# Optimization experiments

Hardware: AMD Instinct MI355X
Metric: run time of the kernel (lower is better)

Reference implementation:

```python
import jax, jax.numpy as jnp
import numpy as np

B, T, C = 1, 2048, 2048
H = 16
DN, DR, DV = 128, 64, 128          # qk_nope_head_dim, qk_rope_head_dim, v_head_dim
QKD = DN + DR                      # 192
RQ, RKV = 1536, 512                # q_lora_rank, kv_lora_rank
EPS = 1e-6
SCALE = QKD ** -0.5


def rmsnorm(v, w):
    return v * jax.lax.rsqrt(jnp.mean(v * v, axis=-1, keepdims=True) + EPS) * w


def rope(x, freqs):
    # x: (B, T, H, d), freqs: (T, d//2) angles. Consecutive-pair complex rotation
    # matching torch view_as_complex(x.reshape(..., -1, 2)) * freqs.
    cos = jnp.cos(freqs)[None, :, None, :]
    sin = jnp.sin(freqs)[None, :, None, :]
    xp = x.reshape(*x.shape[:-1], -1, 2)
    xr, xi = xp[..., 0], xp[..., 1]
    outr = xr * cos - xi * sin
    outi = xr * sin + xi * cos
    return jnp.stack([outr, outi], axis=-1).reshape(x.shape)


def setup_inputs() -> dict:
    key = jax.random.key(0)
    ks = jax.random.split(key, 8)
    s = 0.02
    pos = jnp.arange(T, dtype=jnp.float32)
    inv = 1.0 / (10000.0 ** (jnp.arange(0, DR, 2, dtype=jnp.float32) / DR))  # (DR/2,)
    freqs = pos[:, None] * inv[None, :]  # (T, DR/2) rotation angles
    return {
        "x": jax.random.normal(ks[0], (B, T, C), jnp.float32),
        "freqs": freqs,
        "wq_a": jax.random.normal(ks[1], (RQ, C), jnp.float32) * s,
        "bq_a": jnp.zeros((RQ,), jnp.float32),
        "q_norm_w": jnp.ones((RQ,), jnp.float32),
        "wq_b": jax.random.normal(ks[2], (H * QKD, RQ), jnp.float32) * s,
        "bq_b": jnp.zeros((H * QKD,), jnp.float32),
        "wkv_a": jax.random.normal(ks[3], (RKV + DR, C), jnp.float32) * s,
        "bkv_a": jnp.zeros((RKV + DR,), jnp.float32),
        "kv_norm_w": jnp.ones((RKV,), jnp.float32),
        "wkv_b": jax.random.normal(ks[4], (H * (DN + DV), RKV), jnp.float32) * s,
        "bkv_b": jnp.zeros((H * (DN + DV),), jnp.float32),
        "wo": jax.random.normal(ks[5], (C, C), jnp.float32) * s,
        "bo": jnp.zeros((C,), jnp.float32),
        "prefill": 1,
        "cache_pos": 0,
    }


def reference(x, freqs, wq_a, bq_a, q_norm_w, wq_b, bq_b, wkv_a, bkv_a,
              kv_norm_w, wkv_b, bkv_b, wo, bo, prefill, cache_pos):
    # --- low-rank Q projection ---
    q_lat = rmsnorm(x @ wq_a.T + bq_a, q_norm_w)                 # (B,T,RQ)
    q = (q_lat @ wq_b.T + bq_b).reshape(B, T, H, QKD)
    q_nope, q_pe = q[..., :DN], q[..., DN:]
    q_pe = rope(q_pe, freqs)

    # --- low-rank KV projection ---
    kvpe = x @ wkv_a.T + bkv_a                                   # (B,T,RKV+DR)
    kv_lat, k_pe = kvpe[..., :RKV], kvpe[..., RKV:]
    k_pe = rope(k_pe[:, :, None, :], freqs)                      # (B,T,1,DR)
    kvb = (rmsnorm(kv_lat, kv_norm_w) @ wkv_b.T + bkv_b).reshape(B, T, H, DN + DV)
    k_nope, v = kvb[..., :DN], kvb[..., DN:]

    q = jnp.concatenate([q_nope, q_pe], axis=-1)                 # (B,T,H,QKD)
    k = jnp.concatenate([k_nope, jnp.broadcast_to(k_pe, (B, T, H, DR))], axis=-1)

    # --- causal SDPA (prefill: cache holds exactly the current T tokens) ---
    scores = jnp.einsum('bthd,bshd->bhts', q, k) * SCALE         # (B,H,T,T)
    mask = jnp.tril(jnp.ones((T, T), dtype=bool))
    scores = jnp.where(mask, scores, -jnp.inf)
    att = jax.nn.softmax(scores, axis=-1)
    y = jnp.einsum('bhts,bshd->bthd', att, v).reshape(B, T, C)
    return y @ wo.T + bo
```

## Files before the change

kernel.cpp:

```cpp
#include <hip/hip_runtime.h>
#include <hip/hip_bf16.h>


#define T_DIM 2048
#define H_DIM 16
#define SCALE_F 0.07216878364870322f
#define EPS_F 1e-6f
#define NEG_INF (-3.402823466e38f)

typedef __attribute__((ext_vector_type(8))) short short8;
typedef __attribute__((ext_vector_type(4))) float f32x4;
typedef __attribute__((address_space(3))) char lds_char;
typedef const __attribute__((address_space(1))) char glb_char;

__device__ inline void st_out(float* p, float v) { *p = v; }
__device__ inline void st_out(__hip_bfloat16* p, float v) { *p = __float2bfloat16(v); }

__global__ void cast_bf16_kernel(const float* __restrict__ src,
                                 __hip_bfloat16* __restrict__ dst,
                                 int n4_src, int n4_dst) {
    int i = blockIdx.x * 256 + threadIdx.x;
    if (i >= n4_dst) return;
    float4 v = make_float4(0.f, 0.f, 0.f, 0.f);
    if (i < n4_src) v = ((const float4*)src)[i];
    dst[4 * i + 0] = __float2bfloat16(v.x);
    dst[4 * i + 1] = __float2bfloat16(v.y);
    dst[4 * i + 2] = __float2bfloat16(v.z);
    dst[4 * i + 3] = __float2bfloat16(v.w);
}

__global__ void megacast_kernel(const float* __restrict__ x,
                                const float* __restrict__ wq_a,
                                const float* __restrict__ wkv_a,
                                const float* __restrict__ wq_b,
                                const float* __restrict__ bq_a,
                                const float* __restrict__ bkv_a,
                                __hip_bfloat16* __restrict__ x_bf,
                                __hip_bfloat16* __restrict__ A1,
                                __hip_bfloat16* __restrict__ A2,
                                float* __restrict__ bias_ab) {
    const int i = blockIdx.x * 256 + threadIdx.x;
    float4 v = make_float4(0.f, 0.f, 0.f, 0.f);
    __hip_bfloat16* dst;
    if (i < 1048576) {
        v = ((const float4*)x)[i];            dst = x_bf + 4 * (size_t)i;
    } else if (i < 1835008) {
        int k = i - 1048576;
        v = ((const float4*)wq_a)[k];         dst = A1 + 4 * (size_t)k;
    } else if (i < 2162688) {
        int k = i - 1835008;
        if (k < 294912) v = ((const float4*)wkv_a)[k];
        dst = A1 + (size_t)(786432 + k) * 4;
    } else if (i < 3342336) {
        int k = i - 2162688;
        v = ((const float4*)wq_b)[k];         dst = A2 + 4 * (size_t)k;
    } else if (i < 3342880) {
        int k = i - 3342336;
        float4 b = make_float4(0.f, 0.f, 0.f, 0.f);
        if (k < 384) b = ((const float4*)bq_a)[k];
        else if (k < 528) b = ((const float4*)bkv_a)[k - 384];
        ((float4*)bias_ab)[k] = b;
        return;
    } else return;
    dst[0] = __float2bfloat16(v.x);
    dst[1] = __float2bfloat16(v.y);
    dst[2] = __float2bfloat16(v.z);
    dst[3] = __float2bfloat16(v.w);
}

template <typename OT, bool ROPE>
__global__ __launch_bounds__(512) void gemm_mfma_kernel(
    const __hip_bfloat16* __restrict__ A, int lda,
    const __hip_bfloat16* __restrict__ W, int ldw,
    const float* __restrict__ bias,
    OT* __restrict__ C, int ldc,
    float* __restrict__ C2, int ldc2, int splitN, int K,
    const float* __restrict__ freqs) {
    __shared__ __hip_bfloat16 As[2][128 * 64];
    __shared__ __hip_bfloat16 Bs[2][128 * 64];
    const int tid = threadIdx.x;
    const int w = tid >> 6, lane = tid & 63, qd = lane >> 4, lx = lane & 15;

    const int nwg = gridDim.x * gridDim.y;
    const int o = blockIdx.y * gridDim.x + blockIdx.x;
    const int qx = nwg >> 3, rx = nwg & 7;
    const int xcd = o & 7, idx = o >> 3;
    const int neu = (xcd < rx ? xcd * (qx + 1) : rx * (qx + 1) + (xcd - rx) * qx) + idx;
    const int rowB = (neu / gridDim.x) * 128, colB = (neu % gridDim.x) * 128;

    const int wr = (w >> 1) * 32, wc = (w & 1) * 64;

    f32x4 acc[2][4];
#pragma unroll
    for (int i = 0; i < 2; ++i)
#pragma unroll
        for (int j = 0; j < 4; ++j) acc[i][j] = (f32x4)(0.f);

    auto stage = [&](int buf, int k0) {
#pragma unroll
        for (int it = 0; it < 2; ++it) {
            const int g = tid + it * 512;
            const int row = g >> 3, s = g & 7;
            const int sc = (s ^ (row & 7)) * 8;
            const __hip_bfloat16* ga = A + (size_t)(rowB + row) * lda + k0 + sc;
            __builtin_amdgcn_global_load_lds((glb_char*)ga,
                (lds_char*)((char*)&As[buf][0] + (size_t)g * 16), 16, 0, 0);
            const __hip_bfloat16* gb = W + (size_t)(colB + row) * ldw + k0 + sc;
            __builtin_amdgcn_global_load_lds((glb_char*)gb,
                (lds_char*)((char*)&Bs[buf][0] + (size_t)g * 16), 16, 0, 0);
        }
    };

    stage(0, 0);
    __syncthreads();
    int cur = 0;
    const int swz = (lx & 7) << 4;
    for (int k0 = 0; k0 < K; k0 += 64) {
        if (k0 + 64 < K) stage(cur ^ 1, k0 + 64);

#pragma unroll
        for (int kk = 0; kk < 2; ++kk) {
            short8 a[2], b[4];
#pragma unroll
            for (int rt = 0; rt < 2; ++rt)
                a[rt] = *(const short8*)((char*)&As[cur][0]
                    + (size_t)(wr + rt * 16 + lx) * 128 + ((kk * 64 + qd * 16) ^ swz));
#pragma unroll
            for (int ct = 0; ct < 4; ++ct)
                b[ct] = *(const short8*)((char*)&Bs[cur][0]
                    + (size_t)(wc + ct * 16 + lx) * 128 + ((kk * 64 + qd * 16) ^ swz));
#pragma unroll
            for (int rt = 0; rt < 2; ++rt)
#pragma unroll
                for (int ct = 0; ct < 4; ++ct)
                    acc[rt][ct] = __builtin_amdgcn_mfma_f32_16x16x32_bf16(a[rt], b[ct], acc[rt][ct], 0, 0, 0);
        }
        __syncthreads();
        cur ^= 1;
    }

    const bool second = (C2 != nullptr) && (colB >= splitN);
#pragma unroll
    for (int rt = 0; rt < 2; ++rt)
#pragma unroll
        for (int j = 0; j < 4; ++j) {
            const int row = rowB + wr + rt * 16 + 4 * qd + j;
#pragma unroll
            for (int ct = 0; ct < 4; ++ct) {
                const int col = colB + wc + ct * 16 + lx;
                float v = acc[rt][ct][j] + bias[col];
                if constexpr (ROPE) {
                    const float pv = __shfl_xor(v, 1);
                    const int dm = col % 192;
                    if (dm >= 128) {
                        const int ii = (dm - 128) >> 1;
                        const float f = freqs[row * 32 + ii];
                        const float cc = cosf(f), ss = sinf(f);
                        v = (lane & 1) ? (pv * ss + v * cc)
                                       : (v * cc - pv * ss);
                    }
                }
                if (second) C2[(size_t)row * ldc2 + (col - splitN)] = v;
                else        st_out(&C[(size_t)row * ldc + col], v);
            }
        }
}

__global__ void rmsnorm_kernel(const float* __restrict__ in, __hip_bfloat16* __restrict__ outp,
                               const float* __restrict__ w,
                               int D, int in_stride, int out_stride) {
    const int row = blockIdx.x;
    const float* p = in + (size_t)row * in_stride;
    __hip_bfloat16* o = outp + (size_t)row * out_stride;
    const int tid = threadIdx.x;
    float ss = 0.f;
    for (int i = tid; i < D; i += 256) { float v = p[i]; ss += v * v; }
    __shared__ float red[256];
    red[tid] = ss;
    __syncthreads();
    for (int off = 128; off > 0; off >>= 1) {
        if (tid < off) red[tid] += red[tid + off];
        __syncthreads();
    }
    const float scale = rsqrtf(red[0] / (float)D + EPS_F);
    for (int i = tid; i < D; i += 256)
        o[i] = __float2bfloat16(p[i] * scale * w[i]);
}

__global__ void rmsnorm_rope_kv_kernel(const float* __restrict__ kvpe,
                                       __hip_bfloat16* __restrict__ kv_lat_bf,
                                       const float* __restrict__ w,
                                       const float* __restrict__ freqs,
                                       __hip_bfloat16* __restrict__ kpe) {
    const int row = blockIdx.x;
    const float* p = kvpe + (size_t)row * 640;
    const int tid = threadIdx.x;
    float v0 = p[tid], v1 = p[tid + 256];
    __shared__ float red[256];
    red[tid] = v0 * v0 + v1 * v1;
    __syncthreads();
    for (int off = 128; off > 0; off >>= 1) {
        if (tid < off) red[tid] += red[tid + off];
        __syncthreads();
    }
    const float scale = rsqrtf(red[0] / 512.f + EPS_F);
    __hip_bfloat16* o = kv_lat_bf + (size_t)row * 512;
    o[tid]       = __float2bfloat16(v0 * scale * w[tid]);
    o[tid + 256] = __float2bfloat16(v1 * scale * w[tid + 256]);
    if (tid < 32) {
        const float f = freqs[row * 32 + tid];
        const float c = cosf(f), s = sinf(f);
        const float xr = p[512 + 2 * tid], xi = p[512 + 2 * tid + 1];
        kpe[(size_t)row * 64 + 2 * tid]     = __float2bfloat16(xr * c - xi * s);
        kpe[(size_t)row * 64 + 2 * tid + 1] = __float2bfloat16(xr * s + xi * c);
    }
}

__global__ void pack_vT_kernel(const __hip_bfloat16* __restrict__ kvb,
                               __hip_bfloat16* __restrict__ vT) {
    const int t0 = blockIdx.x * 64;
    const int h = blockIdx.y;
    const int tid = threadIdx.x;
    __shared__ __hip_bfloat16 Ls[64][136];
#pragma unroll
    for (int it = 0; it < 4; ++it) {
        int c = tid + 256 * it;
        int i = c >> 4, part = c & 15;
        *(uint4*)&Ls[i][part * 8] =
            *(const uint4*)(kvb + (size_t)(t0 + i) * 4096 + h * 256 + 128 + part * 8);
    }
    __syncthreads();
#pragma unroll
    for (int it = 0; it < 32; ++it) {
        int c = tid + 256 * it;
        int d = c >> 6, i = c & 63;
        vT[((size_t)(h * 128 + d)) * 2048 + t0 + i] = Ls[i][d];
    }
}

__global__ __launch_bounds__(256) void attn_mfma_kernel(
    const __hip_bfloat16* __restrict__ q,
    const __hip_bfloat16* __restrict__ kv,
    const __hip_bfloat16* __restrict__ kpe,
    const __hip_bfloat16* __restrict__ vT,
    __hip_bfloat16* __restrict__ y) {
    const int o = blockIdx.x;
    const int xcd = o & 7, slot = o >> 3;
    const int h  = xcd * 2 + (slot & 1);
    const int qt = 31 - (slot >> 1);
    const int q0 = qt * 64;
    const int NST = (qt >> 1) + 1;
    const int tid = threadIdx.x;
    const int w = tid >> 6, lane = tid & 63, qd = lane >> 4, lx = lane & 15;

    __shared__ __hip_bfloat16 KsB[128 * 192];
    __shared__ __hip_bfloat16 VsB[128 * 128];
    __shared__ __hip_bfloat16 Ps[4][16][72];

#define KS_ADDR(row, boff) ((char*)KsB + (size_t)(row) * 384 + ((boff) ^ (((row) & 7) << 4)))
#define VS_ADDR(row, boff) ((char*)VsB + (size_t)(row) * 256 + ((boff) ^ (((row) & 7) << 4)))

    short8 qf[6];
    {
        const __hip_bfloat16* qrow =
            q + (size_t)(q0 + 16 * w + lx) * 3072 + h * 192 + qd * 8;
#pragma unroll
        for (int kc = 0; kc < 6; ++kc)
            qf[kc] = *(const short8*)(qrow + kc * 32);
    }

    f32x4 O[8];
#pragma unroll
    for (int i = 0; i < 8; ++i) O[i] = (f32x4)(0.f);
    float mrow[4], lrow[4];
#pragma unroll
    for (int j = 0; j < 4; ++j) { mrow[j] = NEG_INF; lrow[j] = 0.f; }

    const short8 vone = (short8)(short)0x3F80;

    uint4 k0r, k1r, k2r, k3r, k4r, k5r, k6r, k7r;
    uint4 pe0r, pe1r, pe2r, pe3r;
    uint4 v0r, v1r, v2r, v3r, v4r, v5r, v6r, v7r;
    const __hip_bfloat16* kvh = kv + h * 256;
    const __hip_bfloat16* vTh = vT + (size_t)h * 128 * 2048;

#define PREFETCH(S0)                                                               \
    do {                                                                           \
        const size_t kk_ = (size_t)(S0) + (tid >> 4);                              \
        const int kp_ = (tid & 15) * 8;                                            \
        k0r = *(const uint4*)(kvh + (kk_ +   0) * 4096 + kp_);                     \
        k1r = *(const uint4*)(kvh + (kk_ +  16) * 4096 + kp_);                     \
        k2r = *(const uint4*)(kvh + (kk_ +  32) * 4096 + kp_);                     \
        k3r = *(const uint4*)(kvh + (kk_ +  48) * 4096 + kp_);                     \
        k4r = *(const uint4*)(kvh + (kk_ +  64) * 4096 + kp_);                     \
        k5r = *(const uint4*)(kvh + (kk_ +  80) * 4096 + kp_);                     \
        k6r = *(const uint4*)(kvh + (kk_ +  96) * 4096 + kp_);                     \
        k7r = *(const uint4*)(kvh + (kk_ + 112) * 4096 + kp_);                     \
        const size_t pk_ = (size_t)(S0) + (tid >> 3);                              \
        const int pp_ = (tid & 7) * 8;                                             \
        pe0r = *(const uint4*)(kpe + (pk_ +  0) * 64 + pp_);                       \
        pe1r = *(const uint4*)(kpe + (pk_ + 32) * 64 + pp_);                       \
        pe2r = *(const uint4*)(kpe + (pk_ + 64) * 64 + pp_);                       \
        pe3r = *(const uint4*)(kpe + (pk_ + 96) * 64 + pp_);                       \
        const __hip_bfloat16* vp_ = vTh + (size_t)(tid >> 4) * 2048 + (S0) + kp_;  \
        v0r = *(const uint4*)(vp_ + 0 * 32768);                                    \
        v1r = *(const uint4*)(vp_ + 1 * 32768);                                    \
        v2r = *(const uint4*)(vp_ + 2 * 32768);                                    \
        v3r = *(const uint4*)(vp_ + 3 * 32768);                                    \
        v4r = *(const uint4*)(vp_ + 4 * 32768);                                    \
        v5r = *(const uint4*)(vp_ + 5 * 32768);                                    \
        v6r = *(const uint4*)(vp_ + 6 * 32768);                                    \
        v7r = *(const uint4*)(vp_ + 7 * 32768);                                    \
    } while (0)

#define COMPUTE64(S0P, KOFF)                                                       \
    do {                                                                           \
        f32x4 S[4];                                                                \
        _Pragma("unroll")                                                          \
        for (int nt = 0; nt < 4; ++nt) S[nt] = (f32x4)(0.f);                       \
        __builtin_amdgcn_s_setprio(1);                                             \
        _Pragma("unroll")                                                          \
        for (int kc = 0; kc < 6; ++kc) {                                           \
            short8 a = qf[kc];                                                     \
            _Pragma("unroll")                                                      \
            for (int nt = 0; nt < 4; ++nt) {                                       \
                short8 b = *(const short8*)KS_ADDR((KOFF) + nt * 16 + lx,          \
                                                   kc * 64 + qd * 16);             \
                S[nt] = __builtin_amdgcn_mfma_f32_16x16x32_bf16(a, b, S[nt], 0, 0, 0); \
            }                                                                      \
        }                                                                          \
        __builtin_amdgcn_s_setprio(0);                                             \
        float sv[4][4];                                                            \
        _Pragma("unroll")                                                          \
        for (int nt = 0; nt < 4; ++nt) {                                           \
            int col = (S0P) + nt * 16 + lx;                                        \
            _Pragma("unroll")                                                      \
            for (int j = 0; j < 4; ++j) {                                          \
                int row = q0 + 16 * w + 4 * qd + j;                                \
                float v = S[nt][j] * SCALE_F;                                      \
                sv[nt][j] = (col > row) ? NEG_INF : v;                             \
            }                                                                      \
        }                                                                          \
        float pmax[4];                                                             \
        _Pragma("unroll")                                                          \
        for (int j = 0; j < 4; ++j)                                                \
            pmax[j] = fmaxf(fmaxf(sv[0][j], sv[1][j]), fmaxf(sv[2][j], sv[3][j])); \
        const bool need = !__all((pmax[0] <= mrow[0] + 8.f) &&                     \
                                 (pmax[1] <= mrow[1] + 8.f) &&                     \
                                 (pmax[2] <= mrow[2] + 8.f) &&                     \
                                 (pmax[3] <= mrow[3] + 8.f));                      \
        if (need) {                                                                \
            float al[4];                                                           \
            _Pragma("unroll")                                                      \
            for (int j = 0; j < 4; ++j) {                                          \
                float rm = pmax[j];                                                \
                _Pragma("unroll")                                                  \
                for (int msk = 1; msk < 16; msk <<= 1)                             \
                    rm = fmaxf(rm, __shfl_xor(rm, msk));                           \
                const float mn = fmaxf(mrow[j], rm);                               \
                al[j] = __expf(mrow[j] - mn);                                      \
                mrow[j] = mn;                                                      \
                lrow[j] *= al[j];                                                  \
            }                                                                      \
            _Pragma("unroll")                                                      \
            for (int nt = 0; nt < 8; ++nt)                                         \
                _Pragma("unroll")                                                  \
                for (int j = 0; j < 4; ++j) O[nt][j] *= al[j];                     \
        }                                                                          \
        _Pragma("unroll")                                                          \
        for (int nt = 0; nt < 4; ++nt)                                             \
            _Pragma("unroll")                                                      \
            for (int j = 0; j < 4; ++j) {                                          \
                float pp = __expf(sv[nt][j] - mrow[j]);                            \
                Ps[w][4 * qd + j][nt * 16 + lx] = __float2bfloat16(pp);            \
            }                                                                      \
        asm volatile("s_waitcnt lgkmcnt(0)" ::: "memory");                         \
        f32x4 lacc = (f32x4)(0.f);                                                 \
        __builtin_amdgcn_s_setprio(1);                                             \
        _Pragma("unroll")                                                          \
        for (int kc2 = 0; kc2 < 2; ++kc2) {                                        \
            short8 pa = *(const short8*)&Ps[w][lx][kc2 * 32 + qd * 8];             \
            _Pragma("unroll")                                                      \
            for (int nt = 0; nt < 8; ++nt) {                                       \
                short8 vb = *(const short8*)VS_ADDR(nt * 16 + lx,                  \
                                (KOFF) * 2 + kc2 * 64 + qd * 16);                  \
                O[nt] = __builtin_amdgcn_mfma_f32_16x16x32_bf16(pa, vb, O[nt], 0, 0, 0); \
            }                                                                      \
            lacc = __builtin_amdgcn_mfma_f32_16x16x32_bf16(pa, vone, lacc, 0, 0, 0); \
        }                                                                          \
        __builtin_amdgcn_s_setprio(0);                                             \
        _Pragma("unroll")                                                          \
        for (int j = 0; j < 4; ++j) lrow[j] += lacc[j];                            \
    } while (0)

    PREFETCH(0);

    for (int st = 0; st < NST; ++st) {
        const int s0 = st * 128;
        __syncthreads();
        {
            const int kr_ = tid >> 4, kb_ = (tid & 15) * 16;
            *(uint4*)KS_ADDR(kr_ +   0, kb_) = k0r;
            *(uint4*)KS_ADDR(kr_ +  16, kb_) = k1r;
            *(uint4*)KS_ADDR(kr_ +  32, kb_) = k2r;
            *(uint4*)KS_ADDR(kr_ +  48, kb_) = k3r;
            *(uint4*)KS_ADDR(kr_ +  64, kb_) = k4r;
            *(uint4*)KS_ADDR(kr_ +  80, kb_) = k5r;
            *(uint4*)KS_ADDR(kr_ +  96, kb_) = k6r;
            *(uint4*)KS_ADDR(kr_ + 112, kb_) = k7r;
            const int pr_ = tid >> 3, pb_ = (tid & 7) * 16;
            *(uint4*)KS_ADDR(pr_ +  0, 256 + pb_) = pe0r;
            *(uint4*)KS_ADDR(pr_ + 32, 256 + pb_) = pe1r;
            *(uint4*)KS_ADDR(pr_ + 64, 256 + pb_) = pe2r;
            *(uint4*)KS_ADDR(pr_ + 96, 256 + pb_) = pe3r;
            *(uint4*)VS_ADDR(kr_ +   0, kb_) = v0r;
            *(uint4*)VS_ADDR(kr_ +  16, kb_) = v1r;
            *(uint4*)VS_ADDR(kr_ +  32, kb_) = v2r;
            *(uint4*)VS_ADDR(kr_ +  48, kb_) = v3r;
            *(uint4*)VS_ADDR(kr_ +  64, kb_) = v4r;
            *(uint4*)VS_ADDR(kr_ +  80, kb_) = v5r;
            *(uint4*)VS_ADDR(kr_ +  96, kb_) = v6r;
            *(uint4*)VS_ADDR(kr_ + 112, kb_) = v7r;
        }
        __syncthreads();

        if (st + 1 < NST) PREFETCH((st + 1) * 128);

        COMPUTE64(s0, 0);
        if (s0 < q0)
            COMPUTE64(s0 + 64, 64);
    }
#undef PREFETCH
#undef COMPUTE64
#undef KS_ADDR
#undef VS_ADDR

#pragma unroll
    for (int j = 0; j < 4; ++j) {
        const float inv = 1.f / lrow[j];
        const int t = q0 + 16 * w + 4 * qd + j;
        __hip_bfloat16* yr = y + (size_t)t * 2048 + h * 128 + lx;
#pragma unroll
        for (int nt = 0; nt < 8; ++nt) yr[nt * 16] = __float2bfloat16(O[nt][j] * inv);
    }
}

extern "C" void kernel_launch(void* const* d_in, const int* in_sizes, int n_in,
                              void* d_out, int out_size, void* d_ws, size_t ws_size,
                              hipStream_t stream) {
    const float* x         = (const float*)d_in[0];
    const float* freqs     = (const float*)d_in[1];
    const float* wq_a      = (const float*)d_in[2];
    const float* bq_a      = (const float*)d_in[3];
    const float* q_norm_w  = (const float*)d_in[4];
    const float* wq_b      = (const float*)d_in[5];
    const float* bq_b      = (const float*)d_in[6];
    const float* wkv_a     = (const float*)d_in[7];
    const float* bkv_a     = (const float*)d_in[8];
    const float* kv_norm_w = (const float*)d_in[9];
    const float* wkv_b     = (const float*)d_in[10];
    const float* bkv_b     = (const float*)d_in[11];
    const float* wo        = (const float*)d_in[12];
    const float* bo        = (const float*)d_in[13];
    float* out = (float*)d_out;

    char* p = (char*)d_ws;
    float* q_lat = (float*)p;                        p += (size_t)2048 * 1536 * 4;
    float* kvpe  = (float*)p;                        p += (size_t)2048 * 640 * 4;
    __hip_bfloat16* x_bf      = (__hip_bfloat16*)p;  p += (size_t)2048 * 2048 * 2;
    __hip_bfloat16* q_lat_bf  = (__hip_bfloat16*)p;  p += (size_t)2048 * 1536 * 2;
    __hip_bfloat16* qb_bf     = (__hip_bfloat16*)p;  p += (size_t)2048 * 3072 * 2;
    __hip_bfloat16* kv_lat_bf = (__hip_bfloat16*)p;  p += (size_t)2048 * 512 * 2;
    __hip_bfloat16* kvb_bf    = (__hip_bfloat16*)p;  p += (size_t)2048 * 4096 * 2;
    __hip_bfloat16* kpe_bf    = (__hip_bfloat16*)p;  p += (size_t)2048 * 64 * 2;
    __hip_bfloat16* A1        = (__hip_bfloat16*)p;  p += (size_t)3072 * 1536 * 2;
    float* bias_ab = (float*)p;                      p += (size_t)2176 * 4;
    __hip_bfloat16* vT    = x_bf;
    __hip_bfloat16* yb_bf = (__hip_bfloat16*)q_lat;
    __hip_bfloat16* A2    = kvb_bf;

    megacast_kernel<<<13059, 256, 0, stream>>>(x, wq_a, wkv_a, wq_b, bq_a, bkv_a,
                                               x_bf, A1, A2, bias_ab);
    gemm_mfma_kernel<float, false><<<dim3(17, 16), 512, 0, stream>>>(
        x_bf, 2048, A1, 2048, bias_ab, q_lat, 1536, kvpe, 640, 1536, 2048, nullptr);
    cast_bf16_kernel<<<2048, 256, 0, stream>>>(wkv_b, A1, 524288, 524288);
    rmsnorm_kernel<<<2048, 256, 0, stream>>>(q_lat, q_lat_bf, q_norm_w, 1536, 1536, 1536);
    gemm_mfma_kernel<__hip_bfloat16, true><<<dim3(24, 16), 512, 0, stream>>>(
        q_lat_bf, 1536, A2, 1536, bq_b, qb_bf, 3072, nullptr, 0, 1 << 30, 1536, freqs);
    rmsnorm_rope_kv_kernel<<<2048, 256, 0, stream>>>(kvpe, kv_lat_bf, kv_norm_w, freqs, kpe_bf);
    gemm_mfma_kernel<__hip_bfloat16, false><<<dim3(32, 16), 512, 0, stream>>>(
        kv_lat_bf, 512, A1, 512, bkv_b, kvb_bf, 4096, nullptr, 0, 1 << 30, 512, nullptr);
    cast_bf16_kernel<<<4096, 256, 0, stream>>>(wo, A1, 1048576, 1048576);
    pack_vT_kernel<<<dim3(32, 16), 256, 0, stream>>>(kvb_bf, vT);
    attn_mfma_kernel<<<512, 256, 0, stream>>>(qb_bf, kvb_bf, kpe_bf, vT, yb_bf);
    gemm_mfma_kernel<float, false><<<dim3(16, 16), 512, 0, stream>>>(
        yb_bf, 2048, A1, 2048, bo, out, 2048, nullptr, 0, 1 << 30, 2048, nullptr);
}
```

Measured before the change: 355.1 us.

## Split attention KV range across two wave groups and merge partial softmax

The attention kernel now launches 512 threads per block as two groups of four waves. Each group processes alternating 64-key tiles (even or odd) with its own LDS buffers. At the end the two partial results (O, max, sum) are combined through LDS with a log-sum-exp rescale. The goal is to double the waves per query tile and hide latency. The cost is an extra merge step, more register pressure under the 512-thread launch bound, and idle groups on short causal rows.

```diff
diff --git a/kernel.cpp b/kernel.cpp
--- a/kernel.cpp
+++ b/kernel.cpp
@@ -238,7 +238,7 @@
     }
 }
 
-__global__ __launch_bounds__(256) void attn_mfma_kernel(
+__global__ __launch_bounds__(512) void attn_mfma_kernel(
     const __hip_bfloat16* __restrict__ q,
     const __hip_bfloat16* __restrict__ kv,
     const __hip_bfloat16* __restrict__ kpe,
@@ -249,21 +249,23 @@
     const int h  = xcd * 2 + (slot & 1);
     const int qt = 31 - (slot >> 1);
     const int q0 = qt * 64;
-    const int NST = (qt >> 1) + 1;
+    const int NT2 = (qt >> 1) + 1;
     const int tid = threadIdx.x;
-    const int w = tid >> 6, lane = tid & 63, qd = lane >> 4, lx = lane & 15;
-
-    __shared__ __hip_bfloat16 KsB[128 * 192];
-    __shared__ __hip_bfloat16 VsB[128 * 128];
-    __shared__ __hip_bfloat16 Ps[4][16][72];
-
-#define KS_ADDR(row, boff) ((char*)KsB + (size_t)(row) * 384 + ((boff) ^ (((row) & 7) << 4)))
-#define VS_ADDR(row, boff) ((char*)VsB + (size_t)(row) * 256 + ((boff) ^ (((row) & 7) << 4)))
+    const int w = tid >> 6, g = w >> 2, wl = w & 3;
+    const int lane = tid & 63, qd = lane >> 4, lx = lane & 15;
+    const int stid = tid & 255;
+
+    __shared__ __hip_bfloat16 KsB[2][64 * 192];
+    __shared__ __hip_bfloat16 VsB[2][128 * 64];
+    __shared__ __hip_bfloat16 Ps[8][16][72];
+
+#define KS_ADDR(gg, row, boff) ((char*)&KsB[gg][0] + (size_t)(row) * 384 + ((boff) ^ (((row) & 7) << 4)))
+#define VS_ADDR(gg, row, boff) ((char*)&VsB[gg][0] + (size_t)(row) * 128 + ((boff) ^ (((row) & 7) << 4)))
 
     short8 qf[6];
     {
         const __hip_bfloat16* qrow =
-            q + (size_t)(q0 + 16 * w + lx) * 3072 + h * 192 + qd * 8;
+            q + (size_t)(q0 + 16 * wl + lx) * 3072 + h * 192 + qd * 8;
 #pragma unroll
         for (int kc = 0; kc < 6; ++kc)
             qf[kc] = *(const short8*)(qrow + kc * 32);
@@ -278,42 +280,30 @@
 
     const short8 vone = (short8)(short)0x3F80;
 
-    uint4 k0r, k1r, k2r, k3r, k4r, k5r, k6r, k7r;
-    uint4 pe0r, pe1r, pe2r, pe3r;
-    uint4 v0r, v1r, v2r, v3r, v4r, v5r, v6r, v7r;
+    uint4 k0r, k1r, k2r, k3r, pe0r, pe1r, v0r, v1r, v2r, v3r;
     const __hip_bfloat16* kvh = kv + h * 256;
     const __hip_bfloat16* vTh = vT + (size_t)h * 128 * 2048;
 
 #define PREFETCH(S0)                                                               \
     do {                                                                           \
-        const size_t kk_ = (size_t)(S0) + (tid >> 4);                              \
-        const int kp_ = (tid & 15) * 8;                                            \
-        k0r = *(const uint4*)(kvh + (kk_ +   0) * 4096 + kp_);                     \
-        k1r = *(const uint4*)(kvh + (kk_ +  16) * 4096 + kp_);                     \
-        k2r = *(const uint4*)(kvh + (kk_ +  32) * 4096 + kp_);                     \
-        k3r = *(const uint4*)(kvh + (kk_ +  48) * 4096 + kp_);                     \
-        k4r = *(const uint4*)(kvh + (kk_ +  64) * 4096 + kp_);                     \
-        k5r = *(const uint4*)(kvh + (kk_ +  80) * 4096 + kp_);                     \
-        k6r = *(const uint4*)(kvh + (kk_ +  96) * 4096 + kp_);                     \
-        k7r = *(const uint4*)(kvh + (kk_ + 112) * 4096 + kp_);                     \
-        const size_t pk_ = (size_t)(S0) + (tid >> 3);                              \
-        const int pp_ = (tid & 7) * 8;                                             \
+        const size_t kk_ = (size_t)(S0) + (stid >> 4);                             \
+        const int kp_ = (stid & 15) * 8;                                           \
+        k0r = *(const uint4*)(kvh + (kk_ +  0) * 4096 + kp_);                      \
+        k1r = *(const uint4*)(kvh + (kk_ + 16) * 4096 + kp_);                      \
+        k2r = *(const uint4*)(kvh + (kk_ + 32) * 4096 + kp_);                      \
+        k3r = *(const uint4*)(kvh + (kk_ + 48) * 4096 + kp_);                      \
+        const size_t pk_ = (size_t)(S0) + (stid >> 3);                             \
+        const int pp_ = (stid & 7) * 8;                                            \
         pe0r = *(const uint4*)(kpe + (pk_ +  0) * 64 + pp_);                       \
         pe1r = *(const uint4*)(kpe + (pk_ + 32) * 64 + pp_);                       \
-        pe2r = *(const uint4*)(kpe + (pk_ + 64) * 64 + pp_);                       \
-        pe3r = *(const uint4*)(kpe + (pk_ + 96) * 64 + pp_);                       \
-        const __hip_bfloat16* vp_ = vTh + (size_t)(tid >> 4) * 2048 + (S0) + kp_;  \
-        v0r = *(const uint4*)(vp_ + 0 * 32768);                                    \
-        v1r = *(const uint4*)(vp_ + 1 * 32768);                                    \
-        v2r = *(const uint4*)(vp_ + 2 * 32768);                                    \
-        v3r = *(const uint4*)(vp_ + 3 * 32768);                                    \
-        v4r = *(const uint4*)(vp_ + 4 * 32768);                                    \
-        v5r = *(const uint4*)(vp_ + 5 * 32768);                                    \
-        v6r = *(const uint4*)(vp_ + 6 * 32768);                                    \
-        v7r = *(const uint4*)(vp_ + 7 * 32768);                                    \
+        const __hip_bfloat16* vp_ = vTh + ((size_t)(stid >> 3)) * 2048 + (S0) + pp_;\
+        v0r = *(const uint4*)(vp_ + 0 * 65536);                                    \
+        v1r = *(const uint4*)(vp_ + 1 * 65536);                                    \
+        v2r = *(const uint4*)(vp_ + 2 * 65536);                                    \
+        v3r = *(const uint4*)(vp_ + 3 * 65536);                                    \
     } while (0)
 
-#define COMPUTE64(S0P, KOFF)                                                       \
+#define COMPUTE64(S0P, GG)                                                         \
     do {                                                                           \
         f32x4 S[4];                                                                \
         _Pragma("unroll")                                                          \
@@ -324,7 +314,7 @@
             short8 a = qf[kc];                                                     \
             _Pragma("unroll")                                                      \
             for (int nt = 0; nt < 4; ++nt) {                                       \
-                short8 b = *(const short8*)KS_ADDR((KOFF) + nt * 16 + lx,          \
+                short8 b = *(const short8*)KS_ADDR(GG, nt * 16 + lx,               \
                                                    kc * 64 + qd * 16);             \
                 S[nt] = __builtin_amdgcn_mfma_f32_16x16x32_bf16(a, b, S[nt], 0, 0, 0); \
             }                                                                      \
@@ -336,7 +326,7 @@
             int col = (S0P) + nt * 16 + lx;                                        \
             _Pragma("unroll")                                                      \
             for (int j = 0; j < 4; ++j) {                                          \
-                int row = q0 + 16 * w + 4 * qd + j;                                \
+                int row = q0 + 16 * wl + 4 * qd + j;                               \
                 float v = S[nt][j] * SCALE_F;                                      \
                 sv[nt][j] = (col > row) ? NEG_INF : v;                             \
             }                                                                      \
@@ -382,8 +372,8 @@
             short8 pa = *(const short8*)&Ps[w][lx][kc2 * 32 + qd * 8];             \
             _Pragma("unroll")                                                      \
             for (int nt = 0; nt < 8; ++nt) {                                       \
-                short8 vb = *(const short8*)VS_ADDR(nt * 16 + lx,                  \
-                                (KOFF) * 2 + kc2 * 64 + qd * 16);                  \
+                short8 vb = *(const short8*)VS_ADDR(GG, nt * 16 + lx,              \
+                                                    kc2 * 64 + qd * 16);           \
                 O[nt] = __builtin_amdgcn_mfma_f32_16x16x32_bf16(pa, vb, O[nt], 0, 0, 0); \
             }                                                                      \
             lacc = __builtin_amdgcn_mfma_f32_16x16x32_bf16(pa, vone, lacc, 0, 0, 0); \
@@ -393,55 +383,69 @@
         for (int j = 0; j < 4; ++j) lrow[j] += lacc[j];                            \
     } while (0)
 
-    PREFETCH(0);
-
-    for (int st = 0; st < NST; ++st) {
-        const int s0 = st * 128;
+    if (g <= qt) PREFETCH(g * 64);
+
+    for (int t2 = 0; t2 < NT2; ++t2) {
+        const int t = 2 * t2 + g;
+        const bool act = (t <= qt);
         __syncthreads();
-        {
-            const int kr_ = tid >> 4, kb_ = (tid & 15) * 16;
-            *(uint4*)KS_ADDR(kr_ +   0, kb_) = k0r;
-            *(uint4*)KS_ADDR(kr_ +  16, kb_) = k1r;
-            *(uint4*)KS_ADDR(kr_ +  32, kb_) = k2r;
-            *(uint4*)KS_ADDR(kr_ +  48, kb_) = k3r;
-            *(uint4*)KS_ADDR(kr_ +  64, kb_) = k4r;
-            *(uint4*)KS_ADDR(kr_ +  80, kb_) = k5r;
-            *(uint4*)KS_ADDR(kr_ +  96, kb_) = k6r;
-            *(uint4*)KS_ADDR(kr_ + 112, kb_) = k7r;
-            const int pr_ = tid >> 3, pb_ = (tid & 7) * 16;
-            *(uint4*)KS_ADDR(pr_ +  0, 256 + pb_) = pe0r;
-            *(uint4*)KS_ADDR(pr_ + 32, 256 + pb_) = pe1r;
-            *(uint4*)KS_ADDR(pr_ + 64, 256 + pb_) = pe2r;
-            *(uint4*)KS_ADDR(pr_ + 96, 256 + pb_) = pe3r;
-            *(uint4*)VS_ADDR(kr_ +   0, kb_) = v0r;
-            *(uint4*)VS_ADDR(kr_ +  16, kb_) = v1r;
-            *(uint4*)VS_ADDR(kr_ +  32, kb_) = v2r;
-            *(uint4*)VS_ADDR(kr_ +  48, kb_) = v3r;
-            *(uint4*)VS_ADDR(kr_ +  64, kb_) = v4r;
-            *(uint4*)VS_ADDR(kr_ +  80, kb_) = v5r;
-            *(uint4*)VS_ADDR(kr_ +  96, kb_) = v6r;
-            *(uint4*)VS_ADDR(kr_ + 112, kb_) = v7r;
+        if (act) {
+            const int kr_ = stid >> 4, kb_ = (stid & 15) * 16;
+            *(uint4*)KS_ADDR(g, kr_ +  0, kb_) = k0r;
+            *(uint4*)KS_ADDR(g, kr_ + 16, kb_) = k1r;
+            *(uint4*)KS_ADDR(g, kr_ + 32, kb_) = k2r;
+            *(uint4*)KS_ADDR(g, kr_ + 48, kb_) = k3r;
+            const int pr_ = stid >> 3, pb_ = (stid & 7) * 16;
+            *(uint4*)KS_ADDR(g, pr_ +  0, 256 + pb_) = pe0r;
+            *(uint4*)KS_ADDR(g, pr_ + 32, 256 + pb_) = pe1r;
+            *(uint4*)VS_ADDR(g, pr_ +  0, pb_) = v0r;
+            *(uint4*)VS_ADDR(g, pr_ + 32, pb_) = v1r;
+            *(uint4*)VS_ADDR(g, pr_ + 64, pb_) = v2r;
+            *(uint4*)VS_ADDR(g, pr_ + 96, pb_) = v3r;
         }
         __syncthreads();
 
-        if (st + 1 < NST) PREFETCH((st + 1) * 128);
-
-        COMPUTE64(s0, 0);
-        if (s0 < q0)
-            COMPUTE64(s0 + 64, 64);
+        const int tn = 2 * (t2 + 1) + g;
+        if (tn <= qt) PREFETCH(tn * 64);
+
+        if (act) COMPUTE64(t * 64, g);
     }
 #undef PREFETCH
 #undef COMPUTE64
 #undef KS_ADDR
 #undef VS_ADDR
 
-#pragma unroll
-    for (int j = 0; j < 4; ++j) {
-        const float inv = 1.f / lrow[j];
-        const int t = q0 + 16 * w + 4 * qd + j;
-        __hip_bfloat16* yr = y + (size_t)t * 2048 + h * 128 + lx;
-#pragma unroll
-        for (int nt = 0; nt < 8; ++nt) yr[nt * 16] = __float2bfloat16(O[nt][j] * inv);
+    float* Osh = (float*)&KsB[0][0];
+    float* msh = (float*)&VsB[0][0];
+    float* lsh = msh + 64;
+    __syncthreads();
+    if (g == 1) {
+#pragma unroll
+        for (int j = 0; j < 4; ++j) {
+            const int r = 16 * wl + 4 * qd + j;
+            if (lx == 0) { msh[r] = mrow[j]; lsh[r] = lrow[j]; }
+#pragma unroll
+            for (int nt = 0; nt < 8; ++nt)
+                Osh[r * 128 + nt * 16 + lx] = O[nt][j];
+        }
+    }
+    __syncthreads();
+    if (g == 0) {
+#pragma unroll
+        for (int j = 0; j < 4; ++j) {
+            const int r = 16 * wl + 4 * qd + j;
+            const float m1 = msh[r], l1 = lsh[r];
+            const float M  = fmaxf(mrow[j], m1);
+            const float a0 = __expf(mrow[j] - M);
+            const float a1 = __expf(m1 - M);
+            const float inv = 1.f / (lrow[j] * a0 + l1 * a1);
+            const int t = q0 + r;
+            __hip_bfloat16* yr = y + (size_t)t * 2048 + h * 128 + lx;
+#pragma unroll
+            for (int nt = 0; nt < 8; ++nt)
+                yr[nt * 16] = __float2bfloat16(
+                    (O[nt][j] * a0 + Osh[r * 128 + nt * 16 + lx] * a1) * inv);
+        }
     }
 }
 
@@ -492,7 +496,7 @@
         kv_lat_bf, 512, A1, 512, bkv_b, kvb_bf, 4096, nullptr, 0, 1 << 30, 512, nullptr);
     cast_bf16_kernel<<<4096, 256, 0, stream>>>(wo, A1, 1048576, 1048576);
     pack_vT_kernel<<<dim3(32, 16), 256, 0, stream>>>(kvb_bf, vT);
-    attn_mfma_kernel<<<512, 256, 0, stream>>>(qb_bf, kvb_bf, kpe_bf, vT, yb_bf);
+    attn_mfma_kernel<<<512, 512, 0, stream>>>(qb_bf, kvb_bf, kpe_bf, vT, yb_bf);
     gemm_mfma_kernel<float, false><<<dim3(16, 16), 512, 0, stream>>>(
         yb_bf, 2048, A1, 2048, bo, out, 2048, nullptr, 0, 1 << 30, 2048, nullptr);
 }
```

Result: faster. 339.3 us (-4.4%).
